# Kernel tuning notes

Measured on AMD Instinct MI355X. Metric: run time of the kernel, lower is better.

The kernel has to match this reference:

```python
import jax, jax.numpy as jnp
from jax import lax
import numpy as np

# kz = (7, 3): kh is a 1x7 horizontal kernel, kv is a 3x1 vertical kernel
KH = (1, 7)
KV = (3, 1)


def _morph(x, ksz, op, init):
    # F.unfold zero-pads, so padded border values participate in the min/max
    ph, pw = ksz[0] // 2, ksz[1] // 2
    xp = jnp.pad(x, ((0, 0), (0, 0), (ph, ph), (pw, pw)))
    return lax.reduce_window(xp, init, op, (1, 1, ksz[0], ksz[1]), (1, 1, 1, 1), 'VALID')


def _erode(x, ksz):
    return _morph(x, ksz, lax.min, np.float32(np.inf))


def _dilate(x, ksz):
    return _morph(x, ksz, lax.max, np.float32(-np.inf))


def _calphi(x):
    dil = _dilate(x, KH)                                   # horizontal dilation (1x7)
    thr = dil.mean(axis=(2, 3), keepdims=True)             # per-image mean of dilation
    bi = ((x > thr) & (x == dil)).astype(x.dtype)          # horizontal local-max binarization
    return _dilate(_erode(bi, KV), KV)                     # morphological opening with 3x1


def setup_inputs() -> dict:
    key = jax.random.key(0)
    x = jax.random.normal(key, (8, 1, 2048, 2048), dtype=jnp.float32)
    return {"x": x}


def reference(x):
    s1 = _calphi(x).sum()
    s2 = _calphi(jnp.swapaxes(x, 2, 3)).sum()
    return s1 < s2
```

## Files before the change

### kernel.cpp

```cpp
#include <hip/hip_runtime.h>
#include <cstdint>

#define NEG_INF (-__builtin_inff())

static constexpr int H = 2048;
static constexpr int W = 2048;
static constexpr int NIMG = 8;
static constexpr int STR = 248;

struct F4 { float x, y, z, w; };

__device__ __forceinline__ F4 ld4(const float* __restrict__ p) {
    float4 v = *reinterpret_cast<const float4*>(p);
    return {v.x, v.y, v.z, v.w};
}

__device__ __forceinline__ float fmax3(float a, float b, float c) {
    return fmaxf(fmaxf(a, b), c);
}

__device__ __forceinline__ void hmax7_4(float a0, float a1, float a2,
                                        float a3, float a4, float a5, float a6,
                                        float a7, float a8, float a9,
                                        float& m0, float& m1, float& m2, float& m3) {
    float p23 = fmaxf(a2, a3), p45 = fmaxf(a4, a5), p67 = fmaxf(a6, a7);
    float q25 = fmaxf(p23, p45), q47 = fmaxf(p45, p67);
    m0 = fmax3(fmaxf(a0, a1), q25, a6);
    m1 = fmax3(fmaxf(a1, a2), fmax3(a3, a4, a5), fmaxf(a6, a7));
    m2 = fmax3(p23, q47, a8);
    m3 = fmax3(fmaxf(a3, a4), fmax3(a5, a6, a7), fmaxf(a8, a9));
}

template<int RC>
__global__ __launch_bounds__(256) void k_sums(const float* __restrict__ x,
                                              double* __restrict__ sums) {
    const int tid = threadIdx.x;
    const int c4  = blockIdx.x * 1024 + tid * 4;
    const int r0  = blockIdx.y * RC;
    const int b   = blockIdx.z;
    const float* img = x + (size_t)b * H * W;

    const bool laV = (c4 >= 4);
    const bool raV = (c4 + 8 <= W);
    const int  lA  = laV ? (c4 - 4) : 0;
    const int  rA  = raV ? (c4 + 4) : (W - 4);
    const float pad0 = (c4 + 0 < 3 || c4 + 0 > W - 4) ? 0.f : NEG_INF;
    const float pad1 = (c4 + 1 < 3 || c4 + 1 > W - 4) ? 0.f : NEG_INF;
    const float pad2 = (c4 + 2 < 3 || c4 + 2 > W - 4) ? 0.f : NEG_INF;
    const float pad3 = (c4 + 3 < 3 || c4 + 3 > W - 4) ? 0.f : NEG_INF;

    F4 w0, w1, w2, w3, w4, w5, w6;
    w0 = w1 = w2 = w3 = w4 = w5 = w6 = {NEG_INF, NEG_INF, NEG_INF, NEG_INF};
    double sh = 0.0, sv = 0.0;

#pragma unroll
    for (int t = 0; t < RC + 6; ++t) {
        const int ir  = r0 - 3 + t;
        w0 = w1; w1 = w2; w2 = w3; w3 = w4; w4 = w5; w5 = w6;
        const int irc = min(max(ir, 0), H - 1);
        const float* row = img + (size_t)irc * W;
        F4 cur = ld4(row + c4);
        const bool rv = (ir >= 0) && (ir < H);

        if (t >= 3 && t < RC + 3) {
            F4 la = ld4(row + lA);
            F4 ra = ld4(row + rA);
            if (!laV) la = {NEG_INF, NEG_INF, NEG_INF, NEG_INF};
            if (!raV) ra = {NEG_INF, NEG_INF, NEG_INF, NEG_INF};
            float m0, m1, m2, m3;
            hmax7_4(la.y, la.z, la.w, cur.x, cur.y, cur.z, cur.w,
                    ra.x, ra.y, ra.z, m0, m1, m2, m3);
            m0 = fmaxf(m0, pad0); m1 = fmaxf(m1, pad1);
            m2 = fmaxf(m2, pad2); m3 = fmaxf(m3, pad3);
            sh += (double)((m0 + m1) + (m2 + m3));
        }

        F4 cw = cur;
        if (!rv) cw = {NEG_INF, NEG_INF, NEG_INF, NEG_INF};
        w6 = cw;

        const int j = ir - 3;
        if (t >= 6) {
            const float rpad = (j < 3 || j > H - 4) ? 0.f : NEG_INF;
            float mx = fmax3(fmax3(w0.x, w1.x, w2.x), fmax3(w3.x, w4.x, w5.x), w6.x);
            float my = fmax3(fmax3(w0.y, w1.y, w2.y), fmax3(w3.y, w4.y, w5.y), w6.y);
            float mz = fmax3(fmax3(w0.z, w1.z, w2.z), fmax3(w3.z, w4.z, w5.z), w6.z);
            float mw = fmax3(fmax3(w0.w, w1.w, w2.w), fmax3(w3.w, w4.w, w5.w), w6.w);
            mx = fmaxf(mx, rpad); my = fmaxf(my, rpad);
            mz = fmaxf(mz, rpad); mw = fmaxf(mw, rpad);
            sv += (double)((mx + my) + (mz + mw));
        }
    }

    const int lane = tid & 63, wid = tid >> 6;
    for (int off = 32; off > 0; off >>= 1) {
        sh += __shfl_down(sh, off);
        sv += __shfl_down(sv, off);
    }
    __shared__ double sdh[4], sdv[4];
    if (lane == 0) { sdh[wid] = sh; sdv[wid] = sv; }
    __syncthreads();
    if (tid == 0) {
        const int bk = blockIdx.y & 1;
        atomicAdd(&sums[2 * b + bk],      sdh[0] + sdh[1] + sdh[2] + sdh[3]);
        atomicAdd(&sums[16 + 2 * b + bk], sdv[0] + sdv[1] + sdv[2] + sdv[3]);
    }
}

template<int RC>
__global__ __launch_bounds__(256) void k_counts(const float* __restrict__ x,
                                                const double* __restrict__ sums,
                                                unsigned int* __restrict__ cnts) {
    const int tid  = threadIdx.x;
    const int lane = tid & 63;
    const int wid  = tid >> 6;
    const int w    = blockIdx.x * 4 + wid;
    if (w >= 9) return;
    const int cstart = w * STR;
    const int c4   = cstart - 4 + lane * 4;
    const int r0   = blockIdx.y * RC;
    const int b    = blockIdx.z;
    const float* img = x + (size_t)b * H * W;

    const double invHW = 1.0 / ((double)H * (double)W);
    const float thr1 = (float)((sums[2 * b] + sums[2 * b + 1]) * invHW);
    const float thr2 = (float)((sums[16 + 2 * b] + sums[16 + 2 * b + 1]) * invHW);

    int cmask = 0, imask = 0;
#pragma unroll
    for (int k = 0; k < 4; ++k) {
        const int col = c4 + k;
        if (col >= cstart && col < cstart + STR && col < W) cmask |= 1 << k;
        if (col >= 0 && col < W)                            imask |= 1 << k;
    }
    const bool curV = (c4 >= 0) && (c4 <= W - 4);
    const bool laV  = (c4 - 4 >= 0) && (c4 - 4 <= W - 4);
    const bool raV  = (c4 + 4 >= 0) && (c4 + 4 <= W - 4);
    const int cA = min(max(c4, 0), W - 4);
    const int lA = min(max(c4 - 4, 0), W - 4);
    const int rA = min(max(c4 + 4, 0), W - 4);
    const float pad0 = (c4 + 0 < 3 || c4 + 0 > W - 4) ? 0.f : NEG_INF;
    const float pad1 = (c4 + 1 < 3 || c4 + 1 > W - 4) ? 0.f : NEG_INF;
    const float pad2 = (c4 + 2 < 3 || c4 + 2 > W - 4) ? 0.f : NEG_INF;
    const float pad3 = (c4 + 3 < 3 || c4 + 3 > W - 4) ? 0.f : NEG_INF;

    F4 w0, w1, w2, w3, w4, w5, w6;
    w0 = w1 = w2 = w3 = w4 = w5 = w6 = {NEG_INF, NEG_INF, NEG_INF, NEG_INF};
    int bi_m1 = 0, bi_m2 = 0, er_m1 = 0, er_m2 = 0;
    unsigned int cnt1 = 0, cnt2 = 0;

#pragma unroll
    for (int t = 0; t < RC + 6; ++t) {
        const int ir = r0 - 3 + t;
        w0 = w1; w1 = w2; w2 = w3; w3 = w4; w4 = w5; w5 = w6;
        const int irc = min(max(ir, 0), H - 1);
        const float* row = img + (size_t)irc * W;
        F4 cur = ld4(row + cA);
        if (!curV) cur = {NEG_INF, NEG_INF, NEG_INF, NEG_INF};
        const bool rv = (ir >= 0) && (ir < H);

        if (t >= 1 && t <= RC + 4) {
            F4 la = ld4(row + lA);
            F4 ra = ld4(row + rA);
            if (!laV) la = {NEG_INF, NEG_INF, NEG_INF, NEG_INF};
            if (!raV) ra = {NEG_INF, NEG_INF, NEG_INF, NEG_INF};
            float m0, m1, m2, m3;
            hmax7_4(la.y, la.z, la.w, cur.x, cur.y, cur.z, cur.w,
                    ra.x, ra.y, ra.z, m0, m1, m2, m3);
            m0 = fmaxf(m0, pad0); m1 = fmaxf(m1, pad1);
            m2 = fmaxf(m2, pad2); m3 = fmaxf(m3, pad3);
            int bi = ((cur.x > thr1 && cur.x == m0) ? 1 : 0)
                   | ((cur.y > thr1 && cur.y == m1) ? 2 : 0)
                   | ((cur.z > thr1 && cur.z == m2) ? 4 : 0)
                   | ((cur.w > thr1 && cur.w == m3) ? 8 : 0);
            if (!rv) bi = 0;
            const int er = bi_m2 & bi_m1 & bi;
            if (t >= 5) cnt1 += (unsigned int)__popc((er_m2 | er_m1 | er) & cmask);
            er_m2 = er_m1; er_m1 = er;
            bi_m2 = bi_m1; bi_m1 = bi;
        }

        F4 cw = cur;
        if (!rv) cw = {NEG_INF, NEG_INF, NEG_INF, NEG_INF};
        w6 = cw;

        if (t >= 6) {
            const int j = ir - 3;
            const float rpad = (j < 3 || j > H - 4) ? 0.f : NEG_INF;
            float mx = fmax3(fmax3(w0.x, w1.x, w2.x), fmax3(w3.x, w4.x, w5.x), w6.x);
            float my = fmax3(fmax3(w0.y, w1.y, w2.y), fmax3(w3.y, w4.y, w5.y), w6.y);
            float mz = fmax3(fmax3(w0.z, w1.z, w2.z), fmax3(w3.z, w4.z, w5.z), w6.z);
            float mw = fmax3(fmax3(w0.w, w1.w, w2.w), fmax3(w3.w, w4.w, w5.w), w6.w);
            mx = fmaxf(mx, rpad); my = fmaxf(my, rpad);
            mz = fmaxf(mz, rpad); mw = fmaxf(mw, rpad);
            int bi2 = ((w3.x > thr2 && w3.x == mx) ? 1 : 0)
                    | ((w3.y > thr2 && w3.y == my) ? 2 : 0)
                    | ((w3.z > thr2 && w3.z == mz) ? 4 : 0)
                    | ((w3.w > thr2 && w3.w == mw) ? 8 : 0);
            bi2 &= imask;
            const int pb = __shfl_up(bi2, 1);
            const int nb = __shfl_down(bi2, 1);
            const int m6  = (bi2 << 1) | ((pb >> 3) & 1) | ((nb & 1) << 5);
            const int er2 = (m6 & (m6 >> 1) & (m6 >> 2)) & 0xF;
            const int per_ = ((pb >> 2) & (pb >> 3) & bi2) & 1;
            const int ner_ = ((bi2 >> 3) & nb & (nb >> 1)) & 1;
            const int e6 = (er2 << 1) | per_ | (ner_ << 5);
            const int t6 = e6 | (e6 >> 1) | (e6 >> 2);
            cnt2 += (unsigned int)__popc(t6 & cmask);
        }
    }

    for (int off = 32; off > 0; off >>= 1) {
        cnt1 += __shfl_down(cnt1, off);
        cnt2 += __shfl_down(cnt2, off);
    }
    if (lane == 0) {
        const int bkt = (blockIdx.y * 9 + w) & 63;
        atomicAdd(&cnts[bkt],      cnt1);
        atomicAdd(&cnts[64 + bkt], cnt2);
    }
}

__global__ void k_final(const unsigned int* __restrict__ cnts,
                        int* __restrict__ out) {
    const int l = threadIdx.x;
    unsigned int a = cnts[l], c = cnts[64 + l];
    for (int off = 32; off > 0; off >>= 1) {
        a += __shfl_down(a, off);
        c += __shfl_down(c, off);
    }
    if (l == 0) out[0] = (a < c) ? 1 : 0;
}

extern "C" void kernel_launch(void* const* d_in, const int* in_sizes, int n_in,
                              void* d_out, int out_size, void* d_ws, size_t ws_size,
                              hipStream_t stream) {
    const float* x = (const float*)d_in[0];
    int* out = (int*)d_out;
    double* sums = (double*)d_ws;
    unsigned int* cnts = (unsigned int*)((char*)d_ws + 256);

    hipMemsetAsync(d_ws, 0, 1024, stream);

    dim3 blk(256);
    k_sums<16>   <<<dim3(2, 128, 8), blk, 0, stream>>>(x, sums);
    k_counts<16> <<<dim3(3, 128, 8), blk, 0, stream>>>(x, sums, cnts);
    k_final      <<<1, 64, 0, stream>>>(cnts, out);
}
```

Baseline: 273.4 us.

## Preload row tiles into registers and use lane shuffles for horizontal neighbors

Both kernels now have each wave load all 14 rows of its 8-row tile into registers up front. The horizontal 7-wide neighbours come from cross-lane shuffles instead of extra left and right vector loads, and k_sums uses the same overlapping 248-column strip layout as k_counts. The vertical erode and dilate steps work on per-column bitmasks of row flags, and float partial sums are accumulated before the double reduction. A small threshold kernel is added, and atomics are spread over more buckets to reduce contention. The intent is fewer redundant global loads and more memory-level parallelism. The costs are higher register pressure, an extra launch, and slightly more overlap reads at strip edges.

```diff
diff --git a/kernel.cpp b/kernel.cpp
--- a/kernel.cpp
+++ b/kernel.cpp
@@ -5,8 +5,9 @@
 
 static constexpr int H = 2048;
 static constexpr int W = 2048;
-static constexpr int NIMG = 8;
 static constexpr int STR = 248;
+static constexpr int RC  = 8;
+static constexpr int NR  = RC + 6;
 
 struct F4 { float x, y, z, w; };
 
@@ -31,200 +32,222 @@
     m3 = fmax3(fmaxf(a3, a4), fmax3(a5, a6, a7), fmaxf(a8, a9));
 }
 
-template<int RC>
+struct Setup {
+    int c4, cA, cmask, imask;
+    float pad0, pad1, pad2, pad3;
+};
+
+__device__ __forceinline__ Setup make_setup(int sIdx, int lane) {
+    Setup s;
+    const int cstart = sIdx * STR;
+    s.c4 = cstart - 4 + lane * 4;
+    s.cA = min(max(s.c4, 0), W - 4);
+    s.cmask = 0; s.imask = 0;
+#pragma unroll
+    for (int k = 0; k < 4; ++k) {
+        const int col = s.c4 + k;
+        if (col >= cstart && col < cstart + STR && col < W) s.cmask |= 1 << k;
+        if (col >= 0 && col < W)                            s.imask |= 1 << k;
+    }
+    s.pad0 = ((s.c4 + 0) < 3 || (s.c4 + 0) > W - 4) ? 0.f : NEG_INF;
+    s.pad1 = ((s.c4 + 1) < 3 || (s.c4 + 1) > W - 4) ? 0.f : NEG_INF;
+    s.pad2 = ((s.c4 + 2) < 3 || (s.c4 + 2) > W - 4) ? 0.f : NEG_INF;
+    s.pad3 = ((s.c4 + 3) < 3 || (s.c4 + 3) > W - 4) ? 0.f : NEG_INF;
+    return s;
+}
+
+__device__ __forceinline__ void load_rows(const float* __restrict__ img,
+                                          int r0, const Setup& s, F4 (&cur)[NR]) {
+#pragma unroll
+    for (int t = 0; t < NR; ++t) {
+        const int irc = min(max(r0 - 3 + t, 0), H - 1);
+        cur[t] = ld4(img + (size_t)irc * W + s.cA);
+    }
+#pragma unroll
+    for (int t = 0; t < NR; ++t)
+        asm volatile("" : "+v"(cur[t].x), "+v"(cur[t].y), "+v"(cur[t].z), "+v"(cur[t].w));
+    if (s.imask != 0xF) {
+#pragma unroll
+        for (int t = 0; t < NR; ++t) {
+            if (!(s.imask & 1)) cur[t].x = NEG_INF;
+            if (!(s.imask & 2)) cur[t].y = NEG_INF;
+            if (!(s.imask & 4)) cur[t].z = NEG_INF;
+            if (!(s.imask & 8)) cur[t].w = NEG_INF;
+        }
+    }
+#pragma unroll
+    for (int t = 0; t < NR; ++t) {
+        if (t < 3 || t >= NR - 3) {
+            const int ir = r0 - 3 + t;
+            if (ir < 0 || ir >= H) cur[t] = {NEG_INF, NEG_INF, NEG_INF, NEG_INF};
+        }
+    }
+}
+
 __global__ __launch_bounds__(256) void k_sums(const float* __restrict__ x,
                                               double* __restrict__ sums) {
-    const int tid = threadIdx.x;
-    const int c4  = blockIdx.x * 1024 + tid * 4;
-    const int r0  = blockIdx.y * RC;
-    const int b   = blockIdx.z;
+    const int tid = threadIdx.x, lane = tid & 63, wid = tid >> 6;
+    const int sIdx = blockIdx.x;
+    const int rr   = blockIdx.y * 4 + wid;
+    const int b    = blockIdx.z;
+    const int r0   = rr * RC;
     const float* img = x + (size_t)b * H * W;
-
-    const bool laV = (c4 >= 4);
-    const bool raV = (c4 + 8 <= W);
-    const int  lA  = laV ? (c4 - 4) : 0;
-    const int  rA  = raV ? (c4 + 4) : (W - 4);
-    const float pad0 = (c4 + 0 < 3 || c4 + 0 > W - 4) ? 0.f : NEG_INF;
-    const float pad1 = (c4 + 1 < 3 || c4 + 1 > W - 4) ? 0.f : NEG_INF;
-    const float pad2 = (c4 + 2 < 3 || c4 + 2 > W - 4) ? 0.f : NEG_INF;
-    const float pad3 = (c4 + 3 < 3 || c4 + 3 > W - 4) ? 0.f : NEG_INF;
-
-    F4 w0, w1, w2, w3, w4, w5, w6;
-    w0 = w1 = w2 = w3 = w4 = w5 = w6 = {NEG_INF, NEG_INF, NEG_INF, NEG_INF};
-    double sh = 0.0, sv = 0.0;
-
-#pragma unroll
-    for (int t = 0; t < RC + 6; ++t) {
-        const int ir  = r0 - 3 + t;
-        w0 = w1; w1 = w2; w2 = w3; w3 = w4; w4 = w5; w5 = w6;
-        const int irc = min(max(ir, 0), H - 1);
-        const float* row = img + (size_t)irc * W;
-        F4 cur = ld4(row + c4);
-        const bool rv = (ir >= 0) && (ir < H);
-
-        if (t >= 3 && t < RC + 3) {
-            F4 la = ld4(row + lA);
-            F4 ra = ld4(row + rA);
-            if (!laV) la = {NEG_INF, NEG_INF, NEG_INF, NEG_INF};
-            if (!raV) ra = {NEG_INF, NEG_INF, NEG_INF, NEG_INF};
-            float m0, m1, m2, m3;
-            hmax7_4(la.y, la.z, la.w, cur.x, cur.y, cur.z, cur.w,
-                    ra.x, ra.y, ra.z, m0, m1, m2, m3);
-            m0 = fmaxf(m0, pad0); m1 = fmaxf(m1, pad1);
-            m2 = fmaxf(m2, pad2); m3 = fmaxf(m3, pad3);
-            sh += (double)((m0 + m1) + (m2 + m3));
-        }
-
-        F4 cw = cur;
-        if (!rv) cw = {NEG_INF, NEG_INF, NEG_INF, NEG_INF};
-        w6 = cw;
-
-        const int j = ir - 3;
-        if (t >= 6) {
-            const float rpad = (j < 3 || j > H - 4) ? 0.f : NEG_INF;
-            float mx = fmax3(fmax3(w0.x, w1.x, w2.x), fmax3(w3.x, w4.x, w5.x), w6.x);
-            float my = fmax3(fmax3(w0.y, w1.y, w2.y), fmax3(w3.y, w4.y, w5.y), w6.y);
-            float mz = fmax3(fmax3(w0.z, w1.z, w2.z), fmax3(w3.z, w4.z, w5.z), w6.z);
-            float mw = fmax3(fmax3(w0.w, w1.w, w2.w), fmax3(w3.w, w4.w, w5.w), w6.w);
-            mx = fmaxf(mx, rpad); my = fmaxf(my, rpad);
-            mz = fmaxf(mz, rpad); mw = fmaxf(mw, rpad);
-            sv += (double)((mx + my) + (mz + mw));
-        }
-    }
-
-    const int lane = tid & 63, wid = tid >> 6;
+    const Setup s = make_setup(sIdx, lane);
+
+    F4 cur[NR];
+    load_rows(img, r0, s, cur);
+
+    float shf = 0.f, svf = 0.f;
+#pragma unroll
+    for (int t = 3; t < 3 + RC; ++t) {
+        F4 c = cur[t];
+        float la1 = __shfl_up(c.y, 1), la2 = __shfl_up(c.z, 1), la3 = __shfl_up(c.w, 1);
+        float ra0 = __shfl_down(c.x, 1), ra1 = __shfl_down(c.y, 1), ra2 = __shfl_down(c.z, 1);
+        float m0, m1, m2, m3;
+        hmax7_4(la1, la2, la3, c.x, c.y, c.z, c.w, ra0, ra1, ra2, m0, m1, m2, m3);
+        m0 = fmaxf(m0, s.pad0); m1 = fmaxf(m1, s.pad1);
+        m2 = fmaxf(m2, s.pad2); m3 = fmaxf(m3, s.pad3);
+        shf += ((s.cmask & 1) ? m0 : 0.f) + ((s.cmask & 2) ? m1 : 0.f)
+             + ((s.cmask & 4) ? m2 : 0.f) + ((s.cmask & 8) ? m3 : 0.f);
+    }
+#pragma unroll
+    for (int jj = 0; jj < RC; ++jj) {
+        const int j = r0 + jj;
+        const float rpad = (j < 3 || j > H - 4) ? 0.f : NEG_INF;
+        float mx = fmax3(fmax3(cur[jj].x, cur[jj+1].x, cur[jj+2].x),
+                         fmax3(cur[jj+3].x, cur[jj+4].x, cur[jj+5].x), cur[jj+6].x);
+        float my = fmax3(fmax3(cur[jj].y, cur[jj+1].y, cur[jj+2].y),
+                         fmax3(cur[jj+3].y, cur[jj+4].y, cur[jj+5].y), cur[jj+6].y);
+        float mz = fmax3(fmax3(cur[jj].z, cur[jj+1].z, cur[jj+2].z),
+                         fmax3(cur[jj+3].z, cur[jj+4].z, cur[jj+5].z), cur[jj+6].z);
+        float mw = fmax3(fmax3(cur[jj].w, cur[jj+1].w, cur[jj+2].w),
+                         fmax3(cur[jj+3].w, cur[jj+4].w, cur[jj+5].w), cur[jj+6].w);
+        mx = fmaxf(mx, rpad); my = fmaxf(my, rpad);
+        mz = fmaxf(mz, rpad); mw = fmaxf(mw, rpad);
+        svf += ((s.cmask & 1) ? mx : 0.f) + ((s.cmask & 2) ? my : 0.f)
+             + ((s.cmask & 4) ? mz : 0.f) + ((s.cmask & 8) ? mw : 0.f);
+    }
+
+    double sh = (double)shf, sv = (double)svf;
     for (int off = 32; off > 0; off >>= 1) {
         sh += __shfl_down(sh, off);
         sv += __shfl_down(sv, off);
     }
-    __shared__ double sdh[4], sdv[4];
-    if (lane == 0) { sdh[wid] = sh; sdv[wid] = sv; }
-    __syncthreads();
-    if (tid == 0) {
-        const int bk = blockIdx.y & 1;
-        atomicAdd(&sums[2 * b + bk],      sdh[0] + sdh[1] + sdh[2] + sdh[3]);
-        atomicAdd(&sums[16 + 2 * b + bk], sdv[0] + sdv[1] + sdv[2] + sdv[3]);
-    }
-}
-
-template<int RC>
+    if (lane == 0) {
+        const int bk = rr & 63;
+        atomicAdd(&sums[(b)      * 64 + bk], sh);
+        atomicAdd(&sums[(8 + b)  * 64 + bk], sv);
+    }
+}
+
+__global__ void k_thr(const double* __restrict__ sums, float* __restrict__ thr) {
+    const int p = threadIdx.x;
+    if (p < 16) {
+        const double* s = sums + p * 64;
+        double a = 0.0;
+        for (int i = 0; i < 64; ++i) a += s[i];
+        thr[p] = (float)(a * (1.0 / ((double)H * (double)W)));
+    }
+}
+
 __global__ __launch_bounds__(256) void k_counts(const float* __restrict__ x,
-                                                const double* __restrict__ sums,
+                                                const float* __restrict__ thr,
                                                 unsigned int* __restrict__ cnts) {
-    const int tid  = threadIdx.x;
-    const int lane = tid & 63;
-    const int wid  = tid >> 6;
-    const int w    = blockIdx.x * 4 + wid;
-    if (w >= 9) return;
-    const int cstart = w * STR;
-    const int c4   = cstart - 4 + lane * 4;
-    const int r0   = blockIdx.y * RC;
+    const int tid = threadIdx.x, lane = tid & 63, wid = tid >> 6;
+    const int sIdx = blockIdx.x;
+    const int rr   = blockIdx.y * 4 + wid;
     const int b    = blockIdx.z;
+    const int r0   = rr * RC;
     const float* img = x + (size_t)b * H * W;
-
-    const double invHW = 1.0 / ((double)H * (double)W);
-    const float thr1 = (float)((sums[2 * b] + sums[2 * b + 1]) * invHW);
-    const float thr2 = (float)((sums[16 + 2 * b] + sums[16 + 2 * b + 1]) * invHW);
-
-    int cmask = 0, imask = 0;
-#pragma unroll
-    for (int k = 0; k < 4; ++k) {
-        const int col = c4 + k;
-        if (col >= cstart && col < cstart + STR && col < W) cmask |= 1 << k;
-        if (col >= 0 && col < W)                            imask |= 1 << k;
-    }
-    const bool curV = (c4 >= 0) && (c4 <= W - 4);
-    const bool laV  = (c4 - 4 >= 0) && (c4 - 4 <= W - 4);
-    const bool raV  = (c4 + 4 >= 0) && (c4 + 4 <= W - 4);
-    const int cA = min(max(c4, 0), W - 4);
-    const int lA = min(max(c4 - 4, 0), W - 4);
-    const int rA = min(max(c4 + 4, 0), W - 4);
-    const float pad0 = (c4 + 0 < 3 || c4 + 0 > W - 4) ? 0.f : NEG_INF;
-    const float pad1 = (c4 + 1 < 3 || c4 + 1 > W - 4) ? 0.f : NEG_INF;
-    const float pad2 = (c4 + 2 < 3 || c4 + 2 > W - 4) ? 0.f : NEG_INF;
-    const float pad3 = (c4 + 3 < 3 || c4 + 3 > W - 4) ? 0.f : NEG_INF;
-
-    F4 w0, w1, w2, w3, w4, w5, w6;
-    w0 = w1 = w2 = w3 = w4 = w5 = w6 = {NEG_INF, NEG_INF, NEG_INF, NEG_INF};
-    int bi_m1 = 0, bi_m2 = 0, er_m1 = 0, er_m2 = 0;
-    unsigned int cnt1 = 0, cnt2 = 0;
-
-#pragma unroll
-    for (int t = 0; t < RC + 6; ++t) {
-        const int ir = r0 - 3 + t;
-        w0 = w1; w1 = w2; w2 = w3; w3 = w4; w4 = w5; w5 = w6;
-        const int irc = min(max(ir, 0), H - 1);
-        const float* row = img + (size_t)irc * W;
-        F4 cur = ld4(row + cA);
-        if (!curV) cur = {NEG_INF, NEG_INF, NEG_INF, NEG_INF};
-        const bool rv = (ir >= 0) && (ir < H);
-
-        if (t >= 1 && t <= RC + 4) {
-            F4 la = ld4(row + lA);
-            F4 ra = ld4(row + rA);
-            if (!laV) la = {NEG_INF, NEG_INF, NEG_INF, NEG_INF};
-            if (!raV) ra = {NEG_INF, NEG_INF, NEG_INF, NEG_INF};
-            float m0, m1, m2, m3;
-            hmax7_4(la.y, la.z, la.w, cur.x, cur.y, cur.z, cur.w,
-                    ra.x, ra.y, ra.z, m0, m1, m2, m3);
-            m0 = fmaxf(m0, pad0); m1 = fmaxf(m1, pad1);
-            m2 = fmaxf(m2, pad2); m3 = fmaxf(m3, pad3);
-            int bi = ((cur.x > thr1 && cur.x == m0) ? 1 : 0)
-                   | ((cur.y > thr1 && cur.y == m1) ? 2 : 0)
-                   | ((cur.z > thr1 && cur.z == m2) ? 4 : 0)
-                   | ((cur.w > thr1 && cur.w == m3) ? 8 : 0);
-            if (!rv) bi = 0;
-            const int er = bi_m2 & bi_m1 & bi;
-            if (t >= 5) cnt1 += (unsigned int)__popc((er_m2 | er_m1 | er) & cmask);
-            er_m2 = er_m1; er_m1 = er;
-            bi_m2 = bi_m1; bi_m1 = bi;
-        }
-
-        F4 cw = cur;
-        if (!rv) cw = {NEG_INF, NEG_INF, NEG_INF, NEG_INF};
-        w6 = cw;
-
-        if (t >= 6) {
-            const int j = ir - 3;
-            const float rpad = (j < 3 || j > H - 4) ? 0.f : NEG_INF;
-            float mx = fmax3(fmax3(w0.x, w1.x, w2.x), fmax3(w3.x, w4.x, w5.x), w6.x);
-            float my = fmax3(fmax3(w0.y, w1.y, w2.y), fmax3(w3.y, w4.y, w5.y), w6.y);
-            float mz = fmax3(fmax3(w0.z, w1.z, w2.z), fmax3(w3.z, w4.z, w5.z), w6.z);
-            float mw = fmax3(fmax3(w0.w, w1.w, w2.w), fmax3(w3.w, w4.w, w5.w), w6.w);
-            mx = fmaxf(mx, rpad); my = fmaxf(my, rpad);
-            mz = fmaxf(mz, rpad); mw = fmaxf(mw, rpad);
-            int bi2 = ((w3.x > thr2 && w3.x == mx) ? 1 : 0)
-                    | ((w3.y > thr2 && w3.y == my) ? 2 : 0)
-                    | ((w3.z > thr2 && w3.z == mz) ? 4 : 0)
-                    | ((w3.w > thr2 && w3.w == mw) ? 8 : 0);
-            bi2 &= imask;
-            const int pb = __shfl_up(bi2, 1);
-            const int nb = __shfl_down(bi2, 1);
-            const int m6  = (bi2 << 1) | ((pb >> 3) & 1) | ((nb & 1) << 5);
-            const int er2 = (m6 & (m6 >> 1) & (m6 >> 2)) & 0xF;
-            const int per_ = ((pb >> 2) & (pb >> 3) & bi2) & 1;
-            const int ner_ = ((bi2 >> 3) & nb & (nb >> 1)) & 1;
-            const int e6 = (er2 << 1) | per_ | (ner_ << 5);
-            const int t6 = e6 | (e6 >> 1) | (e6 >> 2);
-            cnt2 += (unsigned int)__popc(t6 & cmask);
-        }
-    }
+    const Setup s = make_setup(sIdx, lane);
+    const float thr1 = thr[b], thr2 = thr[8 + b];
+
+    F4 cur[NR];
+    load_rows(img, r0, s, cur);
+
+    unsigned bc0 = 0, bc1 = 0, bc2 = 0, bc3 = 0;
+#pragma unroll
+    for (int t = 1; t < NR - 1; ++t) {
+        F4 c = cur[t];
+        float la1 = __shfl_up(c.y, 1), la2 = __shfl_up(c.z, 1), la3 = __shfl_up(c.w, 1);
+        float ra0 = __shfl_down(c.x, 1), ra1 = __shfl_down(c.y, 1), ra2 = __shfl_down(c.z, 1);
+        float m0, m1, m2, m3;
+        hmax7_4(la1, la2, la3, c.x, c.y, c.z, c.w, ra0, ra1, ra2, m0, m1, m2, m3);
+        m0 = fmaxf(m0, s.pad0); m1 = fmaxf(m1, s.pad1);
+        m2 = fmaxf(m2, s.pad2); m3 = fmaxf(m3, s.pad3);
+        bc0 |= (c.x > thr1 && c.x == m0) ? (1u << t) : 0u;
+        bc1 |= (c.y > thr1 && c.y == m1) ? (1u << t) : 0u;
+        bc2 |= (c.z > thr1 && c.z == m2) ? (1u << t) : 0u;
+        bc3 |= (c.w > thr1 && c.w == m3) ? (1u << t) : 0u;
+    }
+    const unsigned rowm = ((1u << RC) - 1u) << 3;
+    unsigned e0 = bc0 & (bc0 << 1) & (bc0 >> 1);
+    unsigned e1 = bc1 & (bc1 << 1) & (bc1 >> 1);
+    unsigned e2 = bc2 & (bc2 << 1) & (bc2 >> 1);
+    unsigned e3 = bc3 & (bc3 << 1) & (bc3 >> 1);
+    unsigned o0 = e0 | (e0 << 1) | (e0 >> 1);
+    unsigned o1_ = e1 | (e1 << 1) | (e1 >> 1);
+    unsigned o2_ = e2 | (e2 << 1) | (e2 >> 1);
+    unsigned o3_ = e3 | (e3 << 1) | (e3 >> 1);
+    unsigned cnt1 = ((s.cmask & 1) ? __popc(o0  & rowm) : 0u)
+                  + ((s.cmask & 2) ? __popc(o1_ & rowm) : 0u)
+                  + ((s.cmask & 4) ? __popc(o2_ & rowm) : 0u)
+                  + ((s.cmask & 8) ? __popc(o3_ & rowm) : 0u);
+
+    unsigned d0 = 0, d1 = 0, d2 = 0, d3 = 0;
+#pragma unroll
+    for (int jj = 0; jj < RC; ++jj) {
+        const int j = r0 + jj;
+        const float rpad = (j < 3 || j > H - 4) ? 0.f : NEG_INF;
+        float mx = fmax3(fmax3(cur[jj].x, cur[jj+1].x, cur[jj+2].x),
+                         fmax3(cur[jj+3].x, cur[jj+4].x, cur[jj+5].x), cur[jj+6].x);
+        float my = fmax3(fmax3(cur[jj].y, cur[jj+1].y, cur[jj+2].y),
+                         fmax3(cur[jj+3].y, cur[jj+4].y, cur[jj+5].y), cur[jj+6].y);
+        float mz = fmax3(fmax3(cur[jj].z, cur[jj+1].z, cur[jj+2].z),
+                         fmax3(cur[jj+3].z, cur[jj+4].z, cur[jj+5].z), cur[jj+6].z);
+        float mw = fmax3(fmax3(cur[jj].w, cur[jj+1].w, cur[jj+2].w),
+                         fmax3(cur[jj+3].w, cur[jj+4].w, cur[jj+5].w), cur[jj+6].w);
+        mx = fmaxf(mx, rpad); my = fmaxf(my, rpad);
+        mz = fmaxf(mz, rpad); mw = fmaxf(mw, rpad);
+        F4 ce = cur[jj + 3];
+        d0 |= (ce.x > thr2 && ce.x == mx) ? (1u << jj) : 0u;
+        d1 |= (ce.y > thr2 && ce.y == my) ? (1u << jj) : 0u;
+        d2 |= (ce.z > thr2 && ce.z == mz) ? (1u << jj) : 0u;
+        d3 |= (ce.w > thr2 && ce.w == mw) ? (1u << jj) : 0u;
+    }
+    const unsigned pz = __shfl_up(d2, 1), pw = __shfl_up(d3, 1);
+    const unsigned n0 = __shfl_down(d0, 1), n1 = __shfl_down(d1, 1);
+    const unsigned em1 = pz & pw & d0;
+    const unsigned f0  = pw & d0 & d1;
+    const unsigned f1  = d0 & d1 & d2;
+    const unsigned f2  = d1 & d2 & d3;
+    const unsigned f3  = d2 & d3 & n0;
+    const unsigned fp4 = d3 & n0 & n1;
+    const unsigned q0 = em1 | f0 | f1;
+    const unsigned q1 = f0 | f1 | f2;
+    const unsigned q2 = f1 | f2 | f3;
+    const unsigned q3 = f2 | f3 | fp4;
+    unsigned cnt2 = ((s.cmask & 1) ? __popc(q0) : 0u)
+                  + ((s.cmask & 2) ? __popc(q1) : 0u)
+                  + ((s.cmask & 4) ? __popc(q2) : 0u)
+                  + ((s.cmask & 8) ? __popc(q3) : 0u);
 
     for (int off = 32; off > 0; off >>= 1) {
         cnt1 += __shfl_down(cnt1, off);
         cnt2 += __shfl_down(cnt2, off);
     }
     if (lane == 0) {
-        const int bkt = (blockIdx.y * 9 + w) & 63;
-        atomicAdd(&cnts[bkt],      cnt1);
-        atomicAdd(&cnts[64 + bkt], cnt2);
+        const int bkt = (rr * 9 + sIdx) & 127;
+        atomicAdd(&cnts[bkt],       cnt1);
+        atomicAdd(&cnts[128 + bkt], cnt2);
     }
 }
 
 __global__ void k_final(const unsigned int* __restrict__ cnts,
                         int* __restrict__ out) {
     const int l = threadIdx.x;
-    unsigned int a = cnts[l], c = cnts[64 + l];
+    unsigned a = cnts[l] + cnts[64 + l];
+    unsigned c = cnts[128 + l] + cnts[192 + l];
     for (int off = 32; off > 0; off >>= 1) {
         a += __shfl_down(a, off);
         c += __shfl_down(c, off);
@@ -238,12 +261,13 @@
     const float* x = (const float*)d_in[0];
     int* out = (int*)d_out;
     double* sums = (double*)d_ws;
-    unsigned int* cnts = (unsigned int*)((char*)d_ws + 256);
-
-    hipMemsetAsync(d_ws, 0, 1024, stream);
-
-    dim3 blk(256);
-    k_sums<16>   <<<dim3(2, 128, 8), blk, 0, stream>>>(x, sums);
-    k_counts<16> <<<dim3(3, 128, 8), blk, 0, stream>>>(x, sums, cnts);
-    k_final      <<<1, 64, 0, stream>>>(cnts, out);
-}
+    float* thr = (float*)((char*)d_ws + 8192);
+    unsigned int* cnts = (unsigned int*)((char*)d_ws + 8448);
+
+    hipMemsetAsync(d_ws, 0, 16384, stream);
+
+    k_sums  <<<dim3(9, 64, 8), 256, 0, stream>>>(x, sums);
+    k_thr   <<<1, 16, 0, stream>>>(sums, thr);
+    k_counts<<<dim3(9, 64, 8), 256, 0, stream>>>(x, thr, cnts);
+    k_final <<<1, 64, 0, stream>>>(cnts, out);
+}
```

Measured after the change: 247.1 us. 9.6% less time.
